# Kernel tuning notes

Hardware: AMD Instinct MI355X
Metric: run time of the kernel (lower is better)

## Reference

```python
import jax, jax.numpy as jnp
import numpy as np

N0, N1, N2 = 100000, 150000, 80000
E = 1000000
D_IN, D_OUT = 128, 128


def setup_inputs() -> dict:
    key = jax.random.key(0)
    ks = jax.random.split(key, 20)
    s_in = 1.0 / np.sqrt(D_IN)
    s_out = 1.0 / np.sqrt(D_OUT)
    s_agg = 1.0 / np.sqrt(4 * D_OUT)
    return {
        "x0": jax.random.normal(ks[0], (N0, D_IN), jnp.float32),
        "x1": jax.random.normal(ks[1], (N1, D_IN), jnp.float32),
        "x2": jax.random.normal(ks[2], (N2, D_IN), jnp.float32),
        # Linearlayer1: torch Linear(input_size, output_size); stored as (D_IN, D_OUT) => y = x @ W1 + b1
        "W1": jax.random.uniform(ks[3], (D_IN, D_OUT), jnp.float32, -s_in, s_in),
        "b1": jax.random.uniform(ks[4], (D_OUT,), jnp.float32, -s_in, s_in),
        # a_1, a_2: Linear(output_size, 1) -> weight vector (D_OUT,), scalar bias
        "a1_w": jax.random.uniform(ks[5], (D_OUT,), jnp.float32, -s_out, s_out),
        "a1_b": jax.random.uniform(ks[6], (), jnp.float32, -s_out, s_out),
        "a2_w": jax.random.uniform(ks[7], (D_OUT,), jnp.float32, -s_out, s_out),
        "a2_b": jax.random.uniform(ks[8], (), jnp.float32, -s_out, s_out),
        # LinearAgg: Linear(4*output_size, output_size)
        "Wagg": jax.random.uniform(ks[9], (4 * D_OUT, D_OUT), jnp.float32, -s_agg, s_agg),
        "bagg": jax.random.uniform(ks[10], (D_OUT,), jnp.float32, -s_agg, s_agg),
        # sparse incidence matrices as COO edge lists (rows index into n0)
        "adj0_rows": jax.random.randint(ks[11], (E,), 0, N0, jnp.int32),
        "adj0_cols": jax.random.randint(ks[12], (E,), 0, N0, jnp.int32),
        "adj1_rows": jax.random.randint(ks[13], (E,), 0, N0, jnp.int32),
        "adj1_cols": jax.random.randint(ks[14], (E,), 0, N1, jnp.int32),
        "adj2_rows": jax.random.randint(ks[15], (E,), 0, N0, jnp.int32),
        "adj2_cols": jax.random.randint(ks[16], (E,), 0, N2, jnp.int32),
    }


def _attention_agg(xi, xj, rows, cols, a1_w, a1_b, a2_w, a2_b, n_out):
    # edge-wise attention score: sigmoid(a1(xi)[row] + a2(xj)[col]); never build the dense n x n matrix
    a1 = xi @ a1_w + a1_b  # (n_i,)
    a2 = xj @ a2_w + a2_b  # (n_j,)
    att = jax.nn.sigmoid(a1[rows] + a2[cols])  # (E,)
    # sparse.mm(attention, xj): scatter-add att_e * xj[col_e] into row_e
    return jax.ops.segment_sum(att[:, None] * xj[cols], rows, num_segments=n_out)


def reference(x0, x1, x2, W1, b1, a1_w, a1_b, a2_w, a2_b, Wagg, bagg,
              adj0_rows, adj0_cols, adj1_rows, adj1_cols, adj2_rows, adj2_cols):
    lin1 = lambda x: jax.nn.relu(x @ W1 + b1)
    xi_0 = lin1(x0)  # xi_0 == xj_0 in the original (same layer, same input)
    xj_1 = lin1(x1)
    xj_2 = lin1(x2)
    n0 = x0.shape[0]
    agg0 = _attention_agg(xi_0, xi_0, adj0_rows, adj0_cols, a1_w, a1_b, a2_w, a2_b, n0)
    agg1 = _attention_agg(xi_0, xj_1, adj1_rows, adj1_cols, a1_w, a1_b, a2_w, a2_b, n0)
    agg2 = _attention_agg(xi_0, xj_2, adj2_rows, adj2_cols, a1_w, a1_b, a2_w, a2_b, n0)
    cat = jnp.concatenate([xi_0, agg0, agg1, agg2], axis=1)  # (n0, 4*D_OUT)
    return cat @ Wagg + bagg
```

## Files before the change

### kernel.cpp

```cpp
#include <hip/hip_runtime.h>

typedef unsigned int uint32;
typedef unsigned short ushort16;

constexpr int CN0 = 100000;
constexpr int CN1 = 150000;
constexpr int CN2 = 80000;
constexpr int CNE = 1000000;
constexpr int CD  = 128;
constexpr int NBINS = 3 * CN0;
constexpr int TOT_E = 3 * CNE;

constexpr int NB    = (NBINS + 511) / 512;
constexpr int CHUNK = 8192;
constexpr int G     = (TOT_E + CHUNK - 1) / CHUNK;
constexpr int NBG   = NB * G;
constexpr int CSCAN_BLOCKS = (NBG + 1023) / 1024;

constexpr size_t align256(size_t x) { return (x + 255) & ~(size_t)255; }

constexpr size_t OFF_H0B = 0;
constexpr size_t OFF_H1B = align256(OFF_H0B + (size_t)CN0 * CD * 2);
constexpr size_t OFF_H2B = align256(OFF_H1B + (size_t)CN1 * CD * 2);
constexpr size_t OFF_AG1 = align256(OFF_H2B + (size_t)CN2 * CD * 2);
constexpr size_t OFF_AG2 = align256(OFF_AG1 + (size_t)CN0 * CD * 2);
constexpr size_t OFF_A1  = align256(OFF_AG2 + (size_t)CN0 * CD * 2);
constexpr size_t OFF_A2  = align256(OFF_A1 + (size_t)CN0 * 4);
constexpr size_t OFF_RS  = align256(OFF_A2 + (size_t)(CN0 + CN1 + CN2) * 4);
constexpr size_t OFF_BH  = align256(OFF_RS + (size_t)(NBINS + 1) * 4);
constexpr size_t OFF_SCL = align256(OFF_BH + (size_t)NBG * 4);
constexpr size_t OFF_BS  = align256(OFF_SCL + (size_t)TOT_E * 4);
constexpr size_t OFF_BB  = align256(OFF_BS + (size_t)CSCAN_BLOCKS * 4);
constexpr size_t OFF_END = OFF_BB + (size_t)CN0 * CD * 2;

typedef _Float16 f16x2 __attribute__((ext_vector_type(2)));
typedef _Float16 f16x8 __attribute__((ext_vector_type(8)));
typedef __fp16 fp16x2_builtin __attribute__((ext_vector_type(2)));

__device__ inline ushort16 f2h(float f) {
  union { _Float16 h; ushort16 u; } v; v.h = (_Float16)f; return v.u;
}
__device__ inline uint32 packh2(float a, float b) {
  union { fp16x2_builtin h; uint32 u; } v;
  v.h = __builtin_amdgcn_cvt_pkrtz(a, b);
  return v.u;
}

typedef float f32x4 __attribute__((ext_vector_type(4)));
union FragU { uint4 q; f16x8 v; ushort16 u[8]; };

template <int NP, bool RELU, bool DOT1, bool DOT2, typename TA, typename TC>
__global__ __launch_bounds__(256) void gemm_mfma(
    const TA* __restrict__ A0, const TA* __restrict__ A1,
    const TA* __restrict__ A2, const TA* __restrict__ A3,
    const float* __restrict__ W, const float* __restrict__ bias,
    TC* __restrict__ C, int M,
    const float* __restrict__ a1w, const float* __restrict__ a2w,
    const float* __restrict__ a1b, const float* __restrict__ a2b,
    float* __restrict__ dot1out, float* __restrict__ dot2out) {
  constexpr int WS = 136;
  __shared__ ushort16 Wt[128 * WS];

  const int t = threadIdx.x;
  const int wave = t >> 6;
  const int lane = t & 63;
  const int ln = lane & 15;
  const int quad = lane >> 4;
  const int row0 = blockIdx.x * 64;
  const int rowA = row0 + wave * 16 + ln;
  const int rA = (rowA < M) ? rowA : (M - 1);
  const int rowC = row0 + wave * 16 + quad * 4;

  f32x4 acc[8];
#pragma unroll
  for (int j = 0; j < 8; ++j) acc[j] = (f32x4)(0.f);

#pragma unroll
  for (int p = 0; p < NP; ++p) {
    const TA* __restrict__ Ap = (p == 0) ? A0 : ((p == 1) ? A1 : ((p == 2) ? A2 : A3));
    const float* __restrict__ Wp = W + (size_t)p * CD * CD;
    if (p > 0) __syncthreads();
    for (int i = t; i < CD * CD; i += 256) {
      int k = i >> 7, n = i & 127;
      Wt[n * WS + k] = f2h(Wp[i]);
    }
    __syncthreads();
#pragma unroll
    for (int ks = 0; ks < 4; ++ks) {
      const int k0 = ks * 32;
      FragU af;
      if constexpr (sizeof(TA) == 2) {
        af.q = *(const uint4*)((const ushort16*)Ap + (size_t)rA * CD + k0 + quad * 8);
      } else {
        const float* ap = (const float*)Ap + (size_t)rA * CD + k0 + quad * 8;
        float4 f0 = *(const float4*)ap;
        float4 f1 = *(const float4*)(ap + 4);
        af.u[0] = f2h(f0.x); af.u[1] = f2h(f0.y); af.u[2] = f2h(f0.z); af.u[3] = f2h(f0.w);
        af.u[4] = f2h(f1.x); af.u[5] = f2h(f1.y); af.u[6] = f2h(f1.z); af.u[7] = f2h(f1.w);
      }
#pragma unroll
      for (int j = 0; j < 8; ++j) {
        FragU bf;
        bf.q = *(const uint4*)&Wt[(j * 16 + ln) * WS + k0 + quad * 8];
        acc[j] = __builtin_amdgcn_mfma_f32_16x16x32_f16(af.v, bf.v, acc[j], 0, 0, 0);
      }
    }
  }

  float s1[4] = {0.f, 0.f, 0.f, 0.f};
  float s2[4] = {0.f, 0.f, 0.f, 0.f};
#pragma unroll
  for (int j = 0; j < 8; ++j) {
    const int n = j * 16 + ln;
    const float bj = bias[n];
    const float a1wj = DOT1 ? a1w[n] : 0.f;
    const float a2wj = DOT2 ? a2w[n] : 0.f;
#pragma unroll
    for (int r = 0; r < 4; ++r) {
      float v = acc[j][r] + bj;
      if constexpr (RELU) v = fmaxf(v, 0.f);
      const int row = rowC + r;
      if (row < M) {
        if constexpr (sizeof(TC) == 2)
          ((ushort16*)C)[(size_t)row * CD + n] = f2h(v);
        else
          ((float*)C)[(size_t)row * CD + n] = v;
      }
      if constexpr (DOT1) s1[r] = fmaf(v, a1wj, s1[r]);
      if constexpr (DOT2) s2[r] = fmaf(v, a2wj, s2[r]);
    }
  }
  if constexpr (DOT1 || DOT2) {
#pragma unroll
    for (int mask = 1; mask < 16; mask <<= 1) {
#pragma unroll
      for (int r = 0; r < 4; ++r) {
        if constexpr (DOT1) s1[r] += __shfl_xor(s1[r], mask);
        if constexpr (DOT2) s2[r] += __shfl_xor(s2[r], mask);
      }
    }
    if (ln == 0) {
#pragma unroll
      for (int r = 0; r < 4; ++r) {
        const int row = rowC + r;
        if (row < M) {
          if constexpr (DOT2) dot2out[row] = s2[r] + a2b[0];
          if constexpr (DOT1) dot1out[row] = s1[r] + a1b[0];
        }
      }
    }
  }
}

__device__ inline int edge_bin(int e, const int* r0, const int* r1, const int* r2) {
  if (e < CNE) return r0[e];
  if (e < 2 * CNE) return CN0 + r1[e - CNE];
  return 2 * CN0 + r2[e - 2 * CNE];
}
__device__ inline void edge_get(int e, const int* r0, const int* c0, const int* r1,
                                const int* c1, const int* r2, const int* c2,
                                int& bin, int& col) {
  if (e < CNE) { bin = r0[e]; col = c0[e]; }
  else if (e < 2 * CNE) { bin = CN0 + r1[e - CNE]; col = c1[e - CNE]; }
  else { bin = 2 * CN0 + r2[e - 2 * CNE]; col = c2[e - 2 * CNE]; }
}

__global__ __launch_bounds__(256) void coarse_hist_kernel(
    const int* __restrict__ r0, const int* __restrict__ r1, const int* __restrict__ r2,
    int* __restrict__ blockhist) {
  __shared__ int lh[NB];
  const int t = threadIdx.x;
  for (int i = t; i < NB; i += 256) lh[i] = 0;
  __syncthreads();
  const int e0 = blockIdx.x * CHUNK;
  for (int i = t; i < CHUNK; i += 256) {
    int e = e0 + i;
    if (e < TOT_E) atomicAdd(&lh[edge_bin(e, r0, r1, r2) >> 9], 1);
  }
  __syncthreads();
  for (int i = t; i < NB; i += 256) blockhist[(size_t)i * G + blockIdx.x] = lh[i];
}

__global__ void scan1g_kernel(int* __restrict__ data, int* __restrict__ bsums, int n) {
  __shared__ int lds[256];
  int t = threadIdx.x;
  int idx0 = blockIdx.x * 1024 + t * 4;
  int v[4];
#pragma unroll
  for (int j = 0; j < 4; ++j) v[j] = (idx0 + j < n) ? data[idx0 + j] : 0;
  int tsum = v[0] + v[1] + v[2] + v[3];
  lds[t] = tsum;
  __syncthreads();
  for (int off = 1; off < 256; off <<= 1) {
    int x = (t >= off) ? lds[t - off] : 0;
    __syncthreads();
    lds[t] += x;
    __syncthreads();
  }
  int run = lds[t] - tsum;
  if (t == 255) bsums[blockIdx.x] = lds[255];
#pragma unroll
  for (int j = 0; j < 4; ++j) {
    if (idx0 + j < n) data[idx0 + j] = run;
    run += v[j];
  }
}

__global__ void scan2g_kernel(int* __restrict__ bsums, int nb) {
  __shared__ int lds[512];
  int t = threadIdx.x;
  int v = (t < nb) ? bsums[t] : 0;
  lds[t] = v;
  __syncthreads();
  for (int off = 1; off < 512; off <<= 1) {
    int x = (t >= off) ? lds[t - off] : 0;
    __syncthreads();
    lds[t] += x;
    __syncthreads();
  }
  if (t < nb) bsums[t] = lds[t] - v;
}

__global__ void scan3g_kernel(int* __restrict__ data, const int* __restrict__ bsums, int n) {
  int t = threadIdx.x;
  int idx0 = blockIdx.x * 1024 + t * 4;
  int off = bsums[blockIdx.x];
#pragma unroll
  for (int j = 0; j < 4; ++j)
    if (idx0 + j < n) data[idx0 + j] += off;
}

__global__ __launch_bounds__(256) void reorder_kernel(
    const int* __restrict__ r0, const int* __restrict__ c0,
    const int* __restrict__ r1, const int* __restrict__ c1,
    const int* __restrict__ r2, const int* __restrict__ c2,
    const int* __restrict__ blockscan, uint32* __restrict__ bbuf) {
  __shared__ int lbase[NB];
  const int t = threadIdx.x;
  for (int i = t; i < NB; i += 256) lbase[i] = blockscan[(size_t)i * G + blockIdx.x];
  __syncthreads();
  const int e0 = blockIdx.x * CHUNK;
  for (int i = t; i < CHUNK; i += 256) {
    int e = e0 + i;
    if (e >= TOT_E) break;
    int bin, col;
    edge_get(e, r0, c0, r1, c1, r2, c2, bin, col);
    int pos = atomicAdd(&lbase[bin >> 9], 1);
    bbuf[pos] = ((uint32)(bin & 511) << 18) | (uint32)col;
  }
}

__global__ __launch_bounds__(256) void finalize_kernel(
    const int* __restrict__ blockscan, const uint32* __restrict__ bbuf,
    const float* __restrict__ a1_0, const float* __restrict__ a2all,
    uint32* __restrict__ scols, int* __restrict__ rs) {
  __shared__ int lh[512];
  __shared__ int sc[256];
  const int t = threadIdx.x;
  const int b = blockIdx.x;
  const int binbase = b << 9;
  const int gs = blockscan[(size_t)b * G];
  const int ge = (b == NB - 1) ? TOT_E : blockscan[(size_t)(b + 1) * G];
  const int cnt = ge - gs;

  lh[2 * t] = 0;
  lh[2 * t + 1] = 0;
  __syncthreads();
  for (int i = t; i < cnt; i += 256) atomicAdd(&lh[bbuf[gs + i] >> 18], 1);
  __syncthreads();
  int v0 = lh[2 * t], v1 = lh[2 * t + 1];
  int tsum = v0 + v1;
  sc[t] = tsum;
  __syncthreads();
  for (int off = 1; off < 256; off <<= 1) {
    int x = (t >= off) ? sc[t - off] : 0;
    __syncthreads();
    sc[t] += x;
    __syncthreads();
  }
  int ex = sc[t] - tsum;
  lh[2 * t] = ex;
  lh[2 * t + 1] = ex + v0;
  int nb_here = NBINS - binbase;
  if (2 * t < nb_here) rs[binbase + 2 * t] = gs + ex;
  if (2 * t + 1 < nb_here) rs[binbase + 2 * t + 1] = gs + ex + v0;
  if (b == NB - 1 && t == 255) rs[NBINS] = TOT_E;
  __syncthreads();
  for (int i = t; i < cnt; i += 256) {
    uint32 p = bbuf[gs + i];
    int bl = (int)(p >> 18);
    int col = (int)(p & 0x3FFFFu);
    int gbin = binbase + bl;
    int a = (gbin >= 2 * CN0) ? 2 : ((gbin >= CN0) ? 1 : 0);
    int row = gbin - a * CN0;
    int aoff = (a == 0) ? 0 : ((a == 1) ? CN0 : CN0 + CN1);
    float z = a1_0[row] + a2all[aoff + col];
    float att = 1.0f / (1.0f + __expf(-z));
    int q = (int)(att * 16384.f);
    if (q > 16383) q = 16383;
    int pos = atomicAdd(&lh[bl], 1);
    scols[gs + pos] = ((uint32)q << 18) | (uint32)col;
  }
}

__global__ __launch_bounds__(256) void agg_kernel_all(
    const int* __restrict__ rs, const uint32* __restrict__ scols,
    const ushort16* __restrict__ h0,
    const ushort16* __restrict__ h1,
    const ushort16* __restrict__ h2,
    ushort16* __restrict__ agg0, ushort16* __restrict__ agg1,
    ushort16* __restrict__ agg2) {
  const int waveid = (blockIdx.x * blockDim.x + threadIdx.x) >> 6;
  const int g = (threadIdx.x >> 4) & 3;
  const int ln = threadIdx.x & 15;
  const uint32 eoff = (uint32)ln << 4;

  const int w = waveid * 4 + g;
  const bool active = (w < NBINS);
  const int wc = active ? w : (NBINS - 1);

  const int a = (wc >= 2 * CN0) ? 2 : ((wc >= CN0) ? 1 : 0);
  const char* __restrict__ xj =
      (const char*)((a == 0) ? h0 : ((a == 1) ? h1 : h2));
  char* __restrict__ outp = (char*)((a == 0) ? agg0 : ((a == 1) ? agg1 : agg2));
  const int row = wc - a * CN0;

  int s = rs[wc], e = rs[wc + 1];
  if (!active) { s = 0; e = 0; }
  const int pc0 = (e > s) ? (e - 1) : 0;

  constexpr float SC = 1.0f / 16384.f;
  float acc[8];
#pragma unroll
  for (int j = 0; j < 8; ++j) acc[j] = 0.f;

  int mm = e - s;
  mm = max(mm, __shfl_xor(mm, 16));
  mm = max(mm, __shfl_xor(mm, 32));

  int p = s;
  auto round = [&](int q) {
    const int pc = (q < e) ? q : pc0;
    const uint32 k = scols[pc];
    const uint4 v = *(const uint4*)(xj + (((k & 0x3FFFFu) << 8) | eoff));
    const float tv = fmaf((float)(k >> 18), SC, 0.5f * SC);
    const float t = (q < e) ? tv : 0.f;
    union { uint4 q4; f16x2 h[4]; } u;
    u.q4 = v;
    acc[0] = fmaf((float)u.h[0][0], t, acc[0]);
    acc[1] = fmaf((float)u.h[0][1], t, acc[1]);
    acc[2] = fmaf((float)u.h[1][0], t, acc[2]);
    acc[3] = fmaf((float)u.h[1][1], t, acc[3]);
    acc[4] = fmaf((float)u.h[2][0], t, acc[4]);
    acc[5] = fmaf((float)u.h[2][1], t, acc[5]);
    acc[6] = fmaf((float)u.h[3][0], t, acc[6]);
    acc[7] = fmaf((float)u.h[3][1], t, acc[7]);
  };
  for (int i = 0; i < mm; i += 2) {
    round(p);
    round(p + 1);
    p += 2;
  }

  if (active) {
    uint4 o;
    o.x = packh2(acc[0], acc[1]);
    o.y = packh2(acc[2], acc[3]);
    o.z = packh2(acc[4], acc[5]);
    o.w = packh2(acc[6], acc[7]);
    *(uint4*)(outp + (((size_t)row << 8) | eoff)) = o;
  }
}

extern "C" void kernel_launch(void* const* d_in, const int* in_sizes, int n_in,
                              void* d_out, int out_size, void* d_ws, size_t ws_size,
                              hipStream_t stream) {
  const float* x0 = (const float*)d_in[0];
  const float* x1 = (const float*)d_in[1];
  const float* x2 = (const float*)d_in[2];
  const float* W1 = (const float*)d_in[3];
  const float* b1 = (const float*)d_in[4];
  const float* a1_w = (const float*)d_in[5];
  const float* a1_b = (const float*)d_in[6];
  const float* a2_w = (const float*)d_in[7];
  const float* a2_b = (const float*)d_in[8];
  const float* Wagg = (const float*)d_in[9];
  const float* bagg = (const float*)d_in[10];
  const int* adj0_r = (const int*)d_in[11];
  const int* adj0_c = (const int*)d_in[12];
  const int* adj1_r = (const int*)d_in[13];
  const int* adj1_c = (const int*)d_in[14];
  const int* adj2_r = (const int*)d_in[15];
  const int* adj2_c = (const int*)d_in[16];
  float* out = (float*)d_out;

  if (ws_size < OFF_END) return;

  char* ws = (char*)d_ws;
  ushort16* h0b    = (ushort16*)(ws + OFF_H0B);
  ushort16* h1b    = (ushort16*)(ws + OFF_H1B);
  ushort16* h2b    = (ushort16*)(ws + OFF_H2B);
  ushort16* agg1b  = (ushort16*)(ws + OFF_AG1);
  ushort16* agg2b  = (ushort16*)(ws + OFF_AG2);
  float*    a1_0   = (float*)(ws + OFF_A1);
  float*    a2all  = (float*)(ws + OFF_A2);
  int*      rs     = (int*)(ws + OFF_RS);
  int*      bh     = (int*)(ws + OFF_BH);
  uint32*   scols  = (uint32*)(ws + OFF_SCL);
  int*      bsums  = (int*)(ws + OFF_BS);
  uint32*   bbuf   = (uint32*)(ws + OFF_BB);
  ushort16* agg0b  = (ushort16*)(ws + OFF_BB);

  gemm_mfma<1, true, true, true, float, ushort16><<<(CN0 + 63) / 64, 256, 0, stream>>>(
      x0, x0, x0, x0, W1, b1, h0b, CN0, a1_w, a2_w, a1_b, a2_b, a1_0, a2all);
  gemm_mfma<1, true, false, true, float, ushort16><<<(CN1 + 63) / 64, 256, 0, stream>>>(
      x1, x1, x1, x1, W1, b1, h1b, CN1, a1_w, a2_w, a1_b, a2_b, a1_0, a2all + CN0);
  gemm_mfma<1, true, false, true, float, ushort16><<<(CN2 + 63) / 64, 256, 0, stream>>>(
      x2, x2, x2, x2, W1, b1, h2b, CN2, a1_w, a2_w, a1_b, a2_b, a1_0, a2all + CN0 + CN1);

  coarse_hist_kernel<<<G, 256, 0, stream>>>(adj0_r, adj1_r, adj2_r, bh);
  scan1g_kernel<<<CSCAN_BLOCKS, 256, 0, stream>>>(bh, bsums, NBG);
  scan2g_kernel<<<1, 512, 0, stream>>>(bsums, CSCAN_BLOCKS);
  scan3g_kernel<<<CSCAN_BLOCKS, 256, 0, stream>>>(bh, bsums, NBG);
  reorder_kernel<<<G, 256, 0, stream>>>(adj0_r, adj0_c, adj1_r, adj1_c,
                                        adj2_r, adj2_c, bh, bbuf);
  finalize_kernel<<<NB, 256, 0, stream>>>(bh, bbuf, a1_0, a2all, scols, rs);

  {
    const int nwaves = (NBINS + 3) / 4;
    const int nblocks = (nwaves * 64 + 255) / 256;
    agg_kernel_all<<<nblocks, 256, 0, stream>>>(
        rs, scols, h0b, h1b, h2b, agg0b, agg1b, agg2b);
  }

  gemm_mfma<4, false, false, false, ushort16, float><<<(CN0 + 63) / 64, 256, 0, stream>>>(
      h0b, agg0b, agg1b, agg2b, Wagg, bagg, out, CN0,
      a1_w, a2_w, a1_b, a2_b, nullptr, nullptr);
}
```

Baseline: 551.1 us.

## Pretranspose weights to fp16 once and read B fragments from global

```diff
diff --git a/kernel.cpp b/kernel.cpp
--- a/kernel.cpp
+++ b/kernel.cpp
@@ -33,6 +33,7 @@
 constexpr size_t OFF_BB  = align256(OFF_BS + (size_t)CSCAN_BLOCKS * 4);
 constexpr size_t OFF_END = OFF_BB + (size_t)CN0 * CD * 2;
 
+
 typedef _Float16 f16x2 __attribute__((ext_vector_type(2)));
 typedef _Float16 f16x8 __attribute__((ext_vector_type(8)));
 typedef __fp16 fp16x2_builtin __attribute__((ext_vector_type(2)));
@@ -47,20 +48,28 @@
 }
 
 typedef float f32x4 __attribute__((ext_vector_type(4)));
-union FragU { uint4 q; f16x8 v; ushort16 u[8]; };
+union FragU { uint4 q; f16x8 v; ushort16 u[8]; uint32 d[4]; };
+
+__global__ __launch_bounds__(256) void prep_wt1_kernel(
+    const float* __restrict__ W1, ushort16* __restrict__ wt1) {
+  int i = blockIdx.x * 256 + threadIdx.x;
+  if (i < 128 * 128) wt1[i] = f2h(W1[(i & 127) * 128 + (i >> 7)]);
+}
+__global__ __launch_bounds__(256) void prep_wta_kernel(
+    const float* __restrict__ Wagg, ushort16* __restrict__ wta) {
+  int i = blockIdx.x * 256 + threadIdx.x;
+  if (i < 128 * 512) wta[i] = f2h(Wagg[(i & 511) * 128 + (i >> 9)]);
+}
 
 template <int NP, bool RELU, bool DOT1, bool DOT2, typename TA, typename TC>
 __global__ __launch_bounds__(256) void gemm_mfma(
     const TA* __restrict__ A0, const TA* __restrict__ A1,
     const TA* __restrict__ A2, const TA* __restrict__ A3,
-    const float* __restrict__ W, const float* __restrict__ bias,
+    const ushort16* __restrict__ WT, const float* __restrict__ bias,
     TC* __restrict__ C, int M,
     const float* __restrict__ a1w, const float* __restrict__ a2w,
     const float* __restrict__ a1b, const float* __restrict__ a2b,
     float* __restrict__ dot1out, float* __restrict__ dot2out) {
-  constexpr int WS = 136;
-  __shared__ ushort16 Wt[128 * WS];
-
   const int t = threadIdx.x;
   const int wave = t >> 6;
   const int lane = t & 63;
@@ -78,13 +87,6 @@
 #pragma unroll
   for (int p = 0; p < NP; ++p) {
     const TA* __restrict__ Ap = (p == 0) ? A0 : ((p == 1) ? A1 : ((p == 2) ? A2 : A3));
-    const float* __restrict__ Wp = W + (size_t)p * CD * CD;
-    if (p > 0) __syncthreads();
-    for (int i = t; i < CD * CD; i += 256) {
-      int k = i >> 7, n = i & 127;
-      Wt[n * WS + k] = f2h(Wp[i]);
-    }
-    __syncthreads();
 #pragma unroll
     for (int ks = 0; ks < 4; ++ks) {
       const int k0 = ks * 32;
@@ -95,13 +97,13 @@
         const float* ap = (const float*)Ap + (size_t)rA * CD + k0 + quad * 8;
         float4 f0 = *(const float4*)ap;
         float4 f1 = *(const float4*)(ap + 4);
-        af.u[0] = f2h(f0.x); af.u[1] = f2h(f0.y); af.u[2] = f2h(f0.z); af.u[3] = f2h(f0.w);
-        af.u[4] = f2h(f1.x); af.u[5] = f2h(f1.y); af.u[6] = f2h(f1.z); af.u[7] = f2h(f1.w);
+        af.d[0] = packh2(f0.x, f0.y); af.d[1] = packh2(f0.z, f0.w);
+        af.d[2] = packh2(f1.x, f1.y); af.d[3] = packh2(f1.z, f1.w);
       }
 #pragma unroll
       for (int j = 0; j < 8; ++j) {
         FragU bf;
-        bf.q = *(const uint4*)&Wt[(j * 16 + ln) * WS + k0 + quad * 8];
+        bf.q = *(const uint4*)(WT + (size_t)(j * 16 + ln) * (NP * CD) + p * CD + k0 + quad * 8);
         acc[j] = __builtin_amdgcn_mfma_f32_16x16x32_f16(af.v, bf.v, acc[j], 0, 0, 0);
       }
     }
@@ -410,13 +412,17 @@
   int*      bsums  = (int*)(ws + OFF_BS);
   uint32*   bbuf   = (uint32*)(ws + OFF_BB);
   ushort16* agg0b  = (ushort16*)(ws + OFF_BB);
+  ushort16* wt1    = (ushort16*)(ws + OFF_RS);
+  ushort16* wta    = (ushort16*)(ws + OFF_SCL);
+
+  prep_wt1_kernel<<<64, 256, 0, stream>>>(W1, wt1);
 
   gemm_mfma<1, true, true, true, float, ushort16><<<(CN0 + 63) / 64, 256, 0, stream>>>(
-      x0, x0, x0, x0, W1, b1, h0b, CN0, a1_w, a2_w, a1_b, a2_b, a1_0, a2all);
+      x0, x0, x0, x0, wt1, b1, h0b, CN0, a1_w, a2_w, a1_b, a2_b, a1_0, a2all);
   gemm_mfma<1, true, false, true, float, ushort16><<<(CN1 + 63) / 64, 256, 0, stream>>>(
-      x1, x1, x1, x1, W1, b1, h1b, CN1, a1_w, a2_w, a1_b, a2_b, a1_0, a2all + CN0);
+      x1, x1, x1, x1, wt1, b1, h1b, CN1, a1_w, a2_w, a1_b, a2_b, a1_0, a2all + CN0);
   gemm_mfma<1, true, false, true, float, ushort16><<<(CN2 + 63) / 64, 256, 0, stream>>>(
-      x2, x2, x2, x2, W1, b1, h2b, CN2, a1_w, a2_w, a1_b, a2_b, a1_0, a2all + CN0 + CN1);
+      x2, x2, x2, x2, wt1, b1, h2b, CN2, a1_w, a2_w, a1_b, a2_b, a1_0, a2all + CN0 + CN1);
 
   coarse_hist_kernel<<<G, 256, 0, stream>>>(adj0_r, adj1_r, adj2_r, bh);
   scan1g_kernel<<<CSCAN_BLOCKS, 256, 0, stream>>>(bh, bsums, NBG);
@@ -433,7 +439,9 @@
         rs, scols, h0b, h1b, h2b, agg0b, agg1b, agg2b);
   }
 
+  prep_wta_kernel<<<256, 256, 0, stream>>>(Wagg, wta);
+
   gemm_mfma<4, false, false, false, ushort16, float><<<(CN0 + 63) / 64, 256, 0, stream>>>(
-      h0b, agg0b, agg1b, agg2b, Wagg, bagg, out, CN0,
+      h0b, agg0b, agg1b, agg2b, wta, bagg, out, CN0,
       a1_w, a2_w, a1_b, a2_b, nullptr, nullptr);
 }
```

New measurement: 642.0 us. +16.5%, slower.
